# Kernel tuning notes

Hardware: AMD Instinct MI355X
Metric: run time of the kernel (lower is better)

Reference implementation:

```python
import jax, jax.numpy as jnp
import numpy as np

EPS = 1e-12  # F.normalize eps


def setup_inputs() -> dict:
    key = jax.random.key(0)
    ks = jax.random.split(key, 3)
    B, C, D, R = 4096, 32, 128, 8
    return {
        "source": jax.random.normal(ks[0], (B, C, D), dtype=jnp.float32),
        "data": jax.random.normal(ks[1], (B, C, D), dtype=jnp.float32),
        "W": jax.random.normal(ks[2], (R, D, D), dtype=jnp.float32) * (1.0 / np.sqrt(D)),
        "a": jnp.ones((R, C, D), dtype=jnp.float32),
        "c": jnp.ones((R, C, D), dtype=jnp.float32),
        "d": jnp.zeros((R, C, D), dtype=jnp.float32),
    }


def reference(source, data, W, a, c, d):
    # Generate all reflection directions in one batched GEMM:
    # Linear(bias=False): x @ W_r^T, W_r is [out, in]
    v = jnp.einsum("bci,roi->rbco", source, W)          # [R, B, C, D]
    # DynamicTanh: tanh(a*x)*c + d, params [R, C, D] broadcast over batch
    v = jnp.tanh(a[:, None] * v) * c[:, None] + d[:, None]
    # F.normalize(p=2, dim=-1) with eps clamp
    norm = jnp.linalg.norm(v, axis=-1, keepdims=True)
    v = v / jnp.maximum(norm, EPS)

    # Sequential Householder reflections H_R(...H_2(H_1(x)))
    def step(x, vec):
        dot = jnp.sum(vec * x, axis=-1, keepdims=True)  # [B, C, 1]
        return x - 2.0 * vec * dot, None

    out, _ = jax.lax.scan(step, data, v)
    return out
```

## Files before the change

kernel.cpp:

```cpp
#include <hip/hip_runtime.h>
#include <stdint.h>

#define B_DIM 4096
#define C_DIM 32
#define D_DIM 128
#define R_DIM 8
#define BM    128
#define NTHREADS 512

typedef __bf16 bf16x8 __attribute__((ext_vector_type(8)));
typedef float  f32x4  __attribute__((ext_vector_type(4)));

__device__ __forceinline__ uint32_t f2bf(float f) {
  uint32_t u = __float_as_uint(f);
  return (u + 0x7FFFu + ((u >> 16) & 1u)) >> 16;
}

#if __has_builtin(__builtin_amdgcn_exp2f)
#define EXP2F(x) __builtin_amdgcn_exp2f(x)
#else
#define EXP2F(x) exp2f(x)
#endif
#if __has_builtin(__builtin_amdgcn_rcpf)
#define RCPF(x) __builtin_amdgcn_rcpf(x)
#else
#define RCPF(x) (1.0f / (x))
#endif

__device__ __forceinline__ void load_lds16(const void* g, void* l) {
  __builtin_amdgcn_global_load_lds(
      (const __attribute__((address_space(1))) uint32_t*)g,
      (__attribute__((address_space(3))) uint32_t*)l, 16, 0, 0);
}

template <int CTRL>
__device__ __forceinline__ float ror_add(float v) {
  int r = __builtin_amdgcn_update_dpp(0, __builtin_bit_cast(int, v), CTRL, 0xf, 0xf, true);
  return v + __builtin_bit_cast(float, r);
}
__device__ __forceinline__ float red16(float v) {
  v = ror_add<0x128>(v);
  v = ror_add<0x124>(v);
  v = ror_add<0x122>(v);
  v = ror_add<0x121>(v);
  return v;
}

__global__ void prep_w(const float* __restrict__ W, uint32_t* __restrict__ ws) {
  uint32_t t = blockIdx.x * 256u + threadIdx.x;
  uint32_t c  = t >> 2;
  uint32_t j  = t & 3u;
  uint32_t ln = c & 63u;
  uint32_t kt = (c >> 6) & 3u;
  uint32_t n  = (c >> 8) & 7u;
  uint32_t r  = c >> 11;
  uint32_t o  = n * 16u + (ln & 15u);
  uint32_t k  = kt * 32u + (ln >> 4) * 8u + j * 2u;
  const float2 w2 = *reinterpret_cast<const float2*>(
      W + ((size_t)(r * 128u + o)) * 128u + k);
  ws[t] = f2bf(w2.x) | (f2bf(w2.y) << 16);
}

__global__ void prep_acd(const float* __restrict__ A, const float* __restrict__ C,
                         const float* __restrict__ D, float* __restrict__ o) {
  uint32_t t = blockIdx.x * 256u + threadIdx.x;
  uint32_t oo = t & 127u, r = (t >> 7) & 7u, c = t >> 10;
  uint32_t in = (r * 32u + c) * 128u + oo;
  float av = A[in], cv = C[in], dv = D[in];
  uint32_t base = ((c * 8u + r) * 3u) * 128u + oo;
  o[base]       = av * 2.88539008177793f;
  o[base + 128] = -2.f * cv;
  o[base + 256] = cv + dv;
}

__global__ __launch_bounds__(NTHREADS, 4)
void rot_kernel(const float* __restrict__ src, const float* __restrict__ data,
                const uint8_t* __restrict__ wsw, const float* __restrict__ wacd,
                float* __restrict__ out)
{
  __shared__ __align__(16) unsigned char ldsW[65536];
  __shared__ __align__(16) float ldsAcd[R_DIM * 3 * 128];

  const uint32_t tid  = threadIdx.x;
  const uint32_t lane = tid & 63u;
  const uint32_t wid  = tid >> 6;
  const uint32_t l15  = lane & 15u;
  const uint32_t lg   = lane >> 4;

  const uint32_t c0     = blockIdx.x & 31u;
  const uint32_t b_base = (blockIdx.x >> 5) * BM;
  const uint32_t rowb   = b_base + wid * 16u;

  {
    const uint8_t* g = wsw + tid * 16u;
    #pragma unroll
    for (int j = 0; j < 4; ++j)
      load_lds16(g + j * 8192u, &ldsW[wid * 1024u + (uint32_t)j * 8192u]);
  }
  {
    const uint8_t* g = (const uint8_t*)wacd + (uint32_t)c0 * 12288u + tid * 16u;
    load_lds16(g, (uint8_t*)ldsAcd + wid * 1024u);
    if (wid < 4)
      load_lds16(g + 8192u, (uint8_t*)ldsAcd + 8192u + wid * 1024u);
  }

  f32x4 x[8];
  #pragma unroll
  for (int q = 0; q < 4; ++q) {
    const float* xr = data + ((size_t)(rowb + lg * 4 + q) * C_DIM + c0) * D_DIM;
    #pragma unroll
    for (int n = 0; n < 8; ++n) x[n][q] = xr[n * 16 + l15];
  }

  bf16x8 af[4];
  {
    const float* sr = src + ((size_t)(rowb + l15) * C_DIM + c0) * D_DIM + lg * 8u;
    #pragma unroll
    for (int kt = 0; kt < 4; ++kt) {
      float4 f0 = *reinterpret_cast<const float4*>(sr + kt * 32);
      float4 f1 = *reinterpret_cast<const float4*>(sr + kt * 32 + 4);
      union { uint32_t u[4]; bf16x8 v; } p;
      p.u[0] = f2bf(f0.x) | (f2bf(f0.y) << 16);
      p.u[1] = f2bf(f0.z) | (f2bf(f0.w) << 16);
      p.u[2] = f2bf(f1.x) | (f2bf(f1.y) << 16);
      p.u[3] = f2bf(f1.z) | (f2bf(f1.w) << 16);
      af[kt] = p.v;
    }
  }

  __syncthreads();

  for (int r = 0; r < R_DIM; ++r) {
    if (r < 7) {
      const uint8_t* g = wsw + (uint32_t)(r + 1) * 32768u + tid * 16u;
      unsigned char* lb = &ldsW[((r + 1) & 1) * 32768u];
      #pragma unroll
      for (int j = 0; j < 4; ++j)
        load_lds16(g + j * 8192u, &lb[wid * 1024u + (uint32_t)j * 8192u]);
    }

    const uint32_t rb = (r & 1) * 32768u + lane * 16u;
    f32x4 acc[8];
    #pragma unroll
    for (int n = 0; n < 8; ++n) acc[n] = (f32x4){0.f, 0.f, 0.f, 0.f};
    #pragma unroll
    for (int kt = 0; kt < 4; ++kt) {
      #pragma unroll
      for (int nh = 0; nh < 8; nh += 4) {
        bf16x8 bq[4];
        #pragma unroll
        for (int i = 0; i < 4; ++i)
          bq[i] = *reinterpret_cast<const bf16x8*>(
              &ldsW[rb + (uint32_t)(((nh + i) * 4 + kt) * 1024)]);
        #pragma unroll
        for (int i = 0; i < 4; ++i)
          acc[nh + i] = __builtin_amdgcn_mfma_f32_16x16x32_bf16(af[kt], bq[i], acc[nh + i], 0, 0, 0);
      }
    }

    f32x4 s2 = {0.f, 0.f, 0.f, 0.f}, tx = {0.f, 0.f, 0.f, 0.f};
    const float* acdr = ldsAcd + r * 384;
    #pragma unroll
    for (int n = 0; n < 8; ++n) {
      float a2  = acdr[n * 16 + l15];
      float m2c = acdr[128 + n * 16 + l15];
      float cdv = acdr[256 + n * 16 + l15];
      f32x4 z = acc[n] * a2;
      f32x4 ep;
      #pragma unroll
      for (int q = 0; q < 4; ++q) ep[q] = EXP2F(z[q]);
      ep = ep + 1.0f;
      f32x4 pr;
      #pragma unroll
      for (int q = 0; q < 4; ++q) pr[q] = RCPF(ep[q]);
      f32x4 t = pr * m2c + cdv;
      acc[n] = t;
      s2 = s2 + t * t;
      tx = tx + t * x[n];
    }
    #pragma unroll
    for (int q = 0; q < 4; ++q) { s2[q] = red16(s2[q]); tx[q] = red16(tx[q]); }
    f32x4 sc;
    #pragma unroll
    for (int q = 0; q < 4; ++q)
      sc[q] = -2.f * tx[q] * RCPF(fmaxf(s2[q], 1e-24f));
    #pragma unroll
    for (int n = 0; n < 8; ++n)
      x[n] = x[n] + sc * acc[n];

    __syncthreads();
  }

  #pragma unroll
  for (int q = 0; q < 4; ++q) {
    float* orow = out + ((size_t)(rowb + lg * 4 + q) * C_DIM + c0) * D_DIM;
    #pragma unroll
    for (int n = 0; n < 8; ++n) orow[n * 16 + l15] = x[n][q];
  }
}

extern "C" void kernel_launch(void* const* d_in, const int* in_sizes, int n_in,
                              void* d_out, int out_size, void* d_ws, size_t ws_size,
                              hipStream_t stream) {
  const float* src  = (const float*)d_in[0];
  const float* data = (const float*)d_in[1];
  const float* W    = (const float*)d_in[2];
  const float* Aa   = (const float*)d_in[3];
  const float* Cc   = (const float*)d_in[4];
  const float* Dd   = (const float*)d_in[5];
  float* out = (float*)d_out;

  uint8_t* wsW  = (uint8_t*)d_ws;
  float*   wacd = (float*)((uint8_t*)d_ws + 262144);

  prep_w<<<dim3(256), dim3(256), 0, stream>>>(W, (uint32_t*)wsW);
  prep_acd<<<dim3(128), dim3(256), 0, stream>>>(Aa, Cc, Dd, wacd);

  dim3 grid((B_DIM / BM) * C_DIM);
  dim3 block(NTHREADS);
  rot_kernel<<<grid, block, 0, stream>>>(src, data, wsW, wacd, out);
}
```

Baseline: 90.38 us.

## Give each wave two row tiles to reuse W fragments and drop LDS acd staging

Halves the block to 256 threads (4 waves), with each wave now handling two 16-row tiles. Every B fragment read from LDS feeds two MFMAs, which halves LDS reads of W per MFMA. The a/c/d parameters are repacked as float4 per column and read straight from global (L2-cached) each round, replacing the LDS buffer. The cost is higher register pressure (launch bounds drop to 2 blocks per CU) and fewer waves available to hide latency.

```diff
diff --git a/kernel.cpp b/kernel.cpp
--- a/kernel.cpp
+++ b/kernel.cpp
@@ -6,7 +6,7 @@
 #define D_DIM 128
 #define R_DIM 8
 #define BM    128
-#define NTHREADS 512
+#define NTHREADS 256
 
 typedef __bf16 bf16x8 __attribute__((ext_vector_type(8)));
 typedef float  f32x4  __attribute__((ext_vector_type(4)));
@@ -64,22 +64,20 @@
 __global__ void prep_acd(const float* __restrict__ A, const float* __restrict__ C,
                          const float* __restrict__ D, float* __restrict__ o) {
   uint32_t t = blockIdx.x * 256u + threadIdx.x;
-  uint32_t oo = t & 127u, r = (t >> 7) & 7u, c = t >> 10;
-  uint32_t in = (r * 32u + c) * 128u + oo;
+  uint32_t col = t & 127u, r = (t >> 7) & 7u, c = t >> 10;
+  uint32_t in = (r * 32u + c) * 128u + col;
   float av = A[in], cv = C[in], dv = D[in];
-  uint32_t base = ((c * 8u + r) * 3u) * 128u + oo;
-  o[base]       = av * 2.88539008177793f;
-  o[base + 128] = -2.f * cv;
-  o[base + 256] = cv + dv;
-}
-
-__global__ __launch_bounds__(NTHREADS, 4)
+  float4 v = make_float4(av * 2.88539008177793f,
+                         -2.f * cv, cv + dv, 0.f);
+  *reinterpret_cast<float4*>(o + (size_t)t * 4u) = v;
+}
+
+__global__ __launch_bounds__(NTHREADS, 2)
 void rot_kernel(const float* __restrict__ src, const float* __restrict__ data,
                 const uint8_t* __restrict__ wsw, const float* __restrict__ wacd,
                 float* __restrict__ out)
 {
   __shared__ __align__(16) unsigned char ldsW[65536];
-  __shared__ __align__(16) float ldsAcd[R_DIM * 3 * 128];
 
   const uint32_t tid  = threadIdx.x;
   const uint32_t lane = tid & 63u;
@@ -89,32 +87,31 @@
 
   const uint32_t c0     = blockIdx.x & 31u;
   const uint32_t b_base = (blockIdx.x >> 5) * BM;
-  const uint32_t rowb   = b_base + wid * 16u;
+  const uint32_t rowb   = b_base + wid * 32u;
 
   {
-    const uint8_t* g = wsw + tid * 16u;
-    #pragma unroll
-    for (int j = 0; j < 4; ++j)
-      load_lds16(g + j * 8192u, &ldsW[wid * 1024u + (uint32_t)j * 8192u]);
+    #pragma unroll
+    for (int j = 0; j < 8; ++j)
+      load_lds16(wsw + wid * 1024u + (uint32_t)j * 4096u + lane * 16u,
+                 &ldsW[wid * 1024u + (uint32_t)j * 4096u]);
   }
-  {
-    const uint8_t* g = (const uint8_t*)wacd + (uint32_t)c0 * 12288u + tid * 16u;
-    load_lds16(g, (uint8_t*)ldsAcd + wid * 1024u);
-    if (wid < 4)
-      load_lds16(g + 8192u, (uint8_t*)ldsAcd + 8192u + wid * 1024u);
-  }
-
-  f32x4 x[8];
+
+  f32x4 x[2][8];
   #pragma unroll
-  for (int q = 0; q < 4; ++q) {
-    const float* xr = data + ((size_t)(rowb + lg * 4 + q) * C_DIM + c0) * D_DIM;
-    #pragma unroll
-    for (int n = 0; n < 8; ++n) x[n][q] = xr[n * 16 + l15];
-  }
-
-  bf16x8 af[4];
-  {
-    const float* sr = src + ((size_t)(rowb + l15) * C_DIM + c0) * D_DIM + lg * 8u;
+  for (int rt = 0; rt < 2; ++rt)
+    #pragma unroll
+    for (int q = 0; q < 4; ++q) {
+      const float* xr = data +
+          ((size_t)(rowb + rt * 16 + lg * 4 + q) * C_DIM + c0) * D_DIM;
+      #pragma unroll
+      for (int n = 0; n < 8; ++n) x[rt][n][q] = xr[n * 16 + l15];
+    }
+
+  bf16x8 af[2][4];
+  #pragma unroll
+  for (int rt = 0; rt < 2; ++rt) {
+    const float* sr = src +
+        ((size_t)(rowb + rt * 16 + l15) * C_DIM + c0) * D_DIM + lg * 8u;
     #pragma unroll
     for (int kt = 0; kt < 4; ++kt) {
       float4 f0 = *reinterpret_cast<const float4*>(sr + kt * 32);
@@ -124,79 +121,93 @@
       p.u[1] = f2bf(f0.z) | (f2bf(f0.w) << 16);
       p.u[2] = f2bf(f1.x) | (f2bf(f1.y) << 16);
       p.u[3] = f2bf(f1.z) | (f2bf(f1.w) << 16);
-      af[kt] = p.v;
+      af[rt][kt] = p.v;
     }
   }
 
   __syncthreads();
 
   for (int r = 0; r < R_DIM; ++r) {
+    f32x4 acd[8];
+    {
+      const f32x4* g = (const f32x4*)wacd + (uint32_t)(c0 * 8 + r) * 128u + l15;
+      #pragma unroll
+      for (int n = 0; n < 8; ++n) acd[n] = g[n * 16];
+    }
     if (r < 7) {
-      const uint8_t* g = wsw + (uint32_t)(r + 1) * 32768u + tid * 16u;
+      const uint8_t* g = wsw + (uint32_t)(r + 1) * 32768u;
       unsigned char* lb = &ldsW[((r + 1) & 1) * 32768u];
       #pragma unroll
-      for (int j = 0; j < 4; ++j)
-        load_lds16(g + j * 8192u, &lb[wid * 1024u + (uint32_t)j * 8192u]);
+      for (int j = 0; j < 8; ++j)
+        load_lds16(g + wid * 1024u + (uint32_t)j * 4096u + lane * 16u,
+                   &lb[wid * 1024u + (uint32_t)j * 4096u]);
     }
 
     const uint32_t rb = (r & 1) * 32768u + lane * 16u;
-    f32x4 acc[8];
-    #pragma unroll
-    for (int n = 0; n < 8; ++n) acc[n] = (f32x4){0.f, 0.f, 0.f, 0.f};
+    f32x4 acc[2][8];
+    #pragma unroll
+    for (int rt = 0; rt < 2; ++rt)
+      #pragma unroll
+      for (int n = 0; n < 8; ++n) acc[rt][n] = (f32x4){0.f, 0.f, 0.f, 0.f};
     #pragma unroll
     for (int kt = 0; kt < 4; ++kt) {
       #pragma unroll
-      for (int nh = 0; nh < 8; nh += 4) {
-        bf16x8 bq[4];
+      for (int n = 0; n < 8; ++n) {
+        bf16x8 bq = *reinterpret_cast<const bf16x8*>(
+            &ldsW[rb + (uint32_t)((n * 4 + kt) * 1024)]);
+        acc[0][n] = __builtin_amdgcn_mfma_f32_16x16x32_bf16(af[0][kt], bq, acc[0][n], 0, 0, 0);
+        acc[1][n] = __builtin_amdgcn_mfma_f32_16x16x32_bf16(af[1][kt], bq, acc[1][n], 0, 0, 0);
+      }
+    }
+
+    f32x4 s2[2] = {{0.f,0.f,0.f,0.f},{0.f,0.f,0.f,0.f}};
+    f32x4 tx[2] = {{0.f,0.f,0.f,0.f},{0.f,0.f,0.f,0.f}};
+    #pragma unroll
+    for (int rt = 0; rt < 2; ++rt) {
+      #pragma unroll
+      for (int n = 0; n < 8; ++n) {
+        float a2 = acd[n][0], m2c = acd[n][1], cdv = acd[n][2];
+        f32x4 z = acc[rt][n] * a2;
+        f32x4 ep;
         #pragma unroll
-        for (int i = 0; i < 4; ++i)
-          bq[i] = *reinterpret_cast<const bf16x8*>(
-              &ldsW[rb + (uint32_t)(((nh + i) * 4 + kt) * 1024)]);
+        for (int q = 0; q < 4; ++q) ep[q] = EXP2F(z[q]);
+        ep = ep + 1.0f;
+        f32x4 pr;
         #pragma unroll
-        for (int i = 0; i < 4; ++i)
-          acc[nh + i] = __builtin_amdgcn_mfma_f32_16x16x32_bf16(af[kt], bq[i], acc[nh + i], 0, 0, 0);
+        for (int q = 0; q < 4; ++q) pr[q] = RCPF(ep[q]);
+        f32x4 t = pr * m2c + cdv;
+        acc[rt][n] = t;
+        s2[rt] = s2[rt] + t * t;
+        tx[rt] = tx[rt] + t * x[rt][n];
       }
     }
-
-    f32x4 s2 = {0.f, 0.f, 0.f, 0.f}, tx = {0.f, 0.f, 0.f, 0.f};
-    const float* acdr = ldsAcd + r * 384;
-    #pragma unroll
-    for (int n = 0; n < 8; ++n) {
-      float a2  = acdr[n * 16 + l15];
-      float m2c = acdr[128 + n * 16 + l15];
-      float cdv = acdr[256 + n * 16 + l15];
-      f32x4 z = acc[n] * a2;
-      f32x4 ep;
-      #pragma unroll
-      for (int q = 0; q < 4; ++q) ep[q] = EXP2F(z[q]);
-      ep = ep + 1.0f;
-      f32x4 pr;
-      #pragma unroll
-      for (int q = 0; q < 4; ++q) pr[q] = RCPF(ep[q]);
-      f32x4 t = pr * m2c + cdv;
-      acc[n] = t;
-      s2 = s2 + t * t;
-      tx = tx + t * x[n];
-    }
-    #pragma unroll
-    for (int q = 0; q < 4; ++q) { s2[q] = red16(s2[q]); tx[q] = red16(tx[q]); }
-    f32x4 sc;
-    #pragma unroll
-    for (int q = 0; q < 4; ++q)
-      sc[q] = -2.f * tx[q] * RCPF(fmaxf(s2[q], 1e-24f));
-    #pragma unroll
-    for (int n = 0; n < 8; ++n)
-      x[n] = x[n] + sc * acc[n];
+    f32x4 sc[2];
+    #pragma unroll
+    for (int rt = 0; rt < 2; ++rt)
+      #pragma unroll
+      for (int q = 0; q < 4; ++q) {
+        float s = red16(s2[rt][q]);
+        float d = red16(tx[rt][q]);
+        sc[rt][q] = -2.f * d * RCPF(fmaxf(s, 1e-24f));
+      }
+    #pragma unroll
+    for (int rt = 0; rt < 2; ++rt)
+      #pragma unroll
+      for (int n = 0; n < 8; ++n)
+        x[rt][n] = x[rt][n] + sc[rt] * acc[rt][n];
 
     __syncthreads();
   }
 
   #pragma unroll
-  for (int q = 0; q < 4; ++q) {
-    float* orow = out + ((size_t)(rowb + lg * 4 + q) * C_DIM + c0) * D_DIM;
-    #pragma unroll
-    for (int n = 0; n < 8; ++n) orow[n * 16 + l15] = x[n][q];
-  }
+  for (int rt = 0; rt < 2; ++rt)
+    #pragma unroll
+    for (int q = 0; q < 4; ++q) {
+      float* orow = out +
+          ((size_t)(rowb + rt * 16 + lg * 4 + q) * C_DIM + c0) * D_DIM;
+      #pragma unroll
+      for (int n = 0; n < 8; ++n) orow[n * 16 + l15] = x[rt][n][q];
+    }
 }
 
 extern "C" void kernel_launch(void* const* d_in, const int* in_sizes, int n_in,
```

Measured after the change: 97.01 us. +7.3%, slower.
